# Kernel tuning notes

Hardware: AMD Instinct MI355X
Metric: run time of the kernel (lower is better)

The kernel has to match this reference:

```python
import jax, jax.numpy as jnp
import numpy as np

N_GENES = 2000
D_MODEL = 256
N_LAYERS = 4
D_STATE = 16
D_CONV = 4
EXPAND = 2
D_INNER = EXPAND * D_MODEL  # 512
DT_RANK = (D_MODEL + 15) // 16  # 16


def layer_norm(x, w, b, eps=1e-5):
    mu = jnp.mean(x, axis=-1, keepdims=True)
    var = jnp.mean((x - mu) ** 2, axis=-1, keepdims=True)
    return (x - mu) * jax.lax.rsqrt(var + eps) * w + b


def mamba_mixer(h, in_w, cw, cb, xp_w, dtp_w, dtp_b, A_log, Dvec, out_w):
    # h: [B, L, d_model]
    B, L, _ = h.shape
    xz = jnp.einsum('bld,ed->ble', h, in_w)            # [B,L,2*Di]
    u, z = jnp.split(xz, 2, axis=-1)                    # [B,L,Di] each
    # causal depthwise conv1d (kernel D_CONV)
    up = jnp.pad(u, ((0, 0), (D_CONV - 1, 0), (0, 0)))
    u = sum(up[:, k:k + L, :] * cw[:, k] for k in range(D_CONV)) + cb
    u = jax.nn.silu(u)
    # input-dependent dt, B, C
    xdbc = jnp.einsum('bld,ed->ble', u, xp_w)           # [B,L,dt_rank+2N]
    dt_r = xdbc[..., :DT_RANK]
    Bm = xdbc[..., DT_RANK:DT_RANK + D_STATE]           # [B,L,N]
    Cm = xdbc[..., DT_RANK + D_STATE:]                  # [B,L,N]
    dt = jax.nn.softplus(jnp.einsum('blr,dr->bld', dt_r, dtp_w) + dtp_b)  # [B,L,Di]
    A = -jnp.exp(A_log)                                 # [Di,N]
    dA = jnp.exp(dt[..., None] * A)                     # [B,L,Di,N]
    dBu = dt[..., None] * Bm[:, :, None, :] * u[..., None]

    def step(hst, inp):
        a, bu = inp
        hst = a * hst + bu
        return hst, hst

    h0 = jnp.zeros((B, D_INNER, D_STATE), dA.dtype)
    _, hs = jax.lax.scan(step, h0, (jnp.moveaxis(dA, 1, 0), jnp.moveaxis(dBu, 1, 0)))
    y = jnp.einsum('lbdn,lbn->bld', hs, jnp.moveaxis(Cm, 1, 0)) + u * Dvec
    y = y * jax.nn.silu(z)
    return jnp.einsum('bld,ed->ble', y, out_w)          # [B,L,d_model]


def setup_inputs() -> dict:
    key = jax.random.key(0)
    ks = jax.random.split(key, 16)
    nl = N_LAYERS
    inp = {
        'x': jax.random.normal(ks[0], (2, N_GENES), jnp.float32),
        'bulk_in_w': jax.random.normal(ks[1], (D_MODEL,), jnp.float32),
        'bulk_in_b': jnp.zeros((D_MODEL,), jnp.float32),
        'gene_emb': jax.random.normal(ks[2], (1, N_GENES, D_MODEL), jnp.float32) * 0.02,
        'mod_emb': jax.random.normal(ks[3], (1, 1, D_MODEL), jnp.float32) * 0.02,
        'ln_w': jnp.ones((nl, D_MODEL), jnp.float32),
        'ln_b': jnp.zeros((nl, D_MODEL), jnp.float32),
        'in_proj_w': jax.random.normal(ks[4], (nl, 2 * D_INNER, D_MODEL), jnp.float32) * (D_MODEL ** -0.5),
        'conv_w': jax.random.normal(ks[5], (nl, D_INNER, D_CONV), jnp.float32) * (D_CONV ** -0.5),
        'conv_b': jnp.zeros((nl, D_INNER), jnp.float32),
        'x_proj_w': jax.random.normal(ks[6], (nl, DT_RANK + 2 * D_STATE, D_INNER), jnp.float32) * (D_INNER ** -0.5),
        'dt_proj_w': jax.random.normal(ks[7], (nl, D_INNER, DT_RANK), jnp.float32) * 0.01,
        'dt_proj_b': jnp.full((nl, D_INNER), -4.0, jnp.float32),
        'A_log': jnp.broadcast_to(jnp.log(jnp.arange(1, D_STATE + 1, dtype=jnp.float32)), (nl, D_INNER, D_STATE)).copy(),
        'D': jnp.ones((nl, D_INNER), jnp.float32),
        'out_proj_w': jax.random.normal(ks[8], (nl, D_MODEL, D_INNER), jnp.float32) * (D_INNER ** -0.5),
        'fin_w': jnp.ones((D_MODEL,), jnp.float32),
        'fin_b': jnp.zeros((D_MODEL,), jnp.float32),
        'head_w': jax.random.normal(ks[9], (D_MODEL,), jnp.float32) * (D_MODEL ** -0.5),
        'head_b': jnp.zeros((), jnp.float32),
    }
    return inp


def reference(x, bulk_in_w, bulk_in_b, gene_emb, mod_emb, ln_w, ln_b, in_proj_w,
              conv_w, conv_b, x_proj_w, dt_proj_w, dt_proj_b, A_log, D, out_proj_w,
              fin_w, fin_b, head_w, head_b):
    # token embed (modality='bulk'); Linear(1,d_model) == x[...,None]*w + b
    h = x[..., None] * bulk_in_w + bulk_in_b + gene_emb + mod_emb  # [B,L,d_model]
    for i in range(N_LAYERS):
        h = h + mamba_mixer(layer_norm(h, ln_w[i], ln_b[i]), in_proj_w[i], conv_w[i],
                            conv_b[i], x_proj_w[i], dt_proj_w[i], dt_proj_b[i],
                            A_log[i], D[i], out_proj_w[i])
    h = layer_norm(h, fin_w, fin_b)
    y = jnp.einsum('bld,d->bl', h, head_w) + head_b  # bulk head, squeeze(-1)
    return y
```

## Files before the change

kernel.cpp:

```cpp
#include <hip/hip_runtime.h>
#include <math.h>

#define B_  2
#define L_  2000
#define DM_ 256
#define DI_ 512
#define DS_ 16
#define NL_ 4
#define BL_ (B_*L_)
#define BLP_ 4096
#define NC_  125
#define CL_  16
#define NST_ (B_*DI_*DS_)

#define NF_IP_ (NL_*64*8*64)
#define NF_OP_ (NL_*16*16*64)
#define NF_XP_ (NL_*3*16*64)
#define NF_TOT_ (NF_IP_ + NF_OP_ + NF_XP_)

typedef unsigned short ushort_t;
typedef __attribute__((ext_vector_type(8))) short bf16x8;
typedef __attribute__((ext_vector_type(4))) float f32x4;

__device__ __forceinline__ float siluf(float x) { return x / (1.f + __expf(-x)); }
__device__ __forceinline__ ushort_t f2bf(float x) {
    unsigned int u = __float_as_uint(x);
    return (ushort_t)((u + 0x7FFFu + ((u >> 16) & 1u)) >> 16);
}
__device__ __forceinline__ float bf2f(ushort_t v) {
    return __uint_as_float(((unsigned int)v) << 16);
}

__global__ __launch_bounds__(256) void embed_f2bf_kernel(
    const float* __restrict__ x, const float* __restrict__ biw,
    const float* __restrict__ bib, const float* __restrict__ ge,
    const float* __restrict__ me, const float* __restrict__ lnw,
    const float* __restrict__ lnb,
    float* __restrict__ h, ushort_t* __restrict__ aln,
    const float* __restrict__ ipw, const float* __restrict__ opw,
    const float* __restrict__ xpw, ushort_t* __restrict__ ipwb,
    ushort_t* __restrict__ opwb, ushort_t* __restrict__ xpwb)
{
    if (blockIdx.x < BL_) {
        __shared__ float sm[8];
        int bl = blockIdx.x, d = threadIdx.x;
        int l = bl % L_;
        float v = x[bl]*biw[d] + bib[d] + ge[(size_t)l*DM_ + d] + me[d];
        h[(size_t)bl*DM_ + d] = v;
        float s = v, q = v*v;
        #pragma unroll
        for (int o = 32; o > 0; o >>= 1) {
            s += __shfl_down(s, o);
            q += __shfl_down(q, o);
        }
        if ((d & 63) == 0) { sm[d >> 6] = s; sm[4 + (d >> 6)] = q; }
        __syncthreads();
        float sum = sm[0]+sm[1]+sm[2]+sm[3];
        float ssq = sm[4]+sm[5]+sm[6]+sm[7];
        float mu  = sum * (1.f/DM_);
        float inv = rsqrtf(fmaxf(ssq*(1.f/DM_) - mu*mu, 0.f) + 1e-5f);
        aln[(size_t)bl*DM_ + d] = f2bf((v - mu)*inv*lnw[d] + lnb[d]);
    } else {
        int i = (blockIdx.x - BL_)*256 + threadIdx.x;
        if (i >= NF_TOT_) return;
        const float* src; ushort_t* dst;
        if (i < NF_IP_) {
            int f = i;
            int li   = f >> 15;
            int r    = f & 32767;
            int t    = r >> 9;
            int rem  = r & 511;
            int ks   = rem >> 6;
            int lane = rem & 63;
            src = ipw + ((size_t)(li*1024 + t*16 + (lane & 15)))*DM_
                      + ks*32 + (lane >> 4)*8;
            dst = ipwb + (size_t)f*8;
        } else if (i < NF_IP_ + NF_OP_) {
            int f = i - NF_IP_;
            int li   = f >> 14;
            int r    = f & 16383;
            int t    = r >> 10;
            int rem  = r & 1023;
            int ks   = rem >> 6;
            int lane = rem & 63;
            src = opw + ((size_t)(li*256 + t*16 + (lane & 15)))*DI_
                      + ks*32 + (lane >> 4)*8;
            dst = opwb + (size_t)f*8;
        } else {
            int f = i - NF_IP_ - NF_OP_;
            int li   = f / 3072;
            int r    = f % 3072;
            int t    = r >> 10;
            int rem  = r & 1023;
            int ks   = rem >> 6;
            int lane = rem & 63;
            src = xpw + ((size_t)(li*48 + t*16 + (lane & 15)))*DI_
                      + ks*32 + (lane >> 4)*8;
            dst = xpwb + (size_t)f*8;
        }
        float4 v0 = *(const float4*)src;
        float4 v1 = *(const float4*)(src + 4);
        __align__(16) ushort_t o[8];
        o[0] = f2bf(v0.x); o[1] = f2bf(v0.y); o[2] = f2bf(v0.z); o[3] = f2bf(v0.w);
        o[4] = f2bf(v1.x); o[5] = f2bf(v1.y); o[6] = f2bf(v1.z); o[7] = f2bf(v1.w);
        *(uint4*)dst = *(const uint4*)o;
    }
}

__global__ __launch_bounds__(256) void gemm_bf(
    const ushort_t* __restrict__ A, const ushort_t* __restrict__ Wp,
    ushort_t* __restrict__ C)
{
    __shared__ ushort_t a_s[128*64];
    const int r0 = blockIdx.x*128, c0 = blockIdx.y*128;
    const int tid = threadIdx.x;
    const int lane = tid & 63, w = tid >> 6;
    const int wm = (w & 1)*64, wn = (w >> 1)*64;
    const int qd = lane >> 4, l16 = lane & 15;
    const int tb = (c0 + wn) >> 4;
    f32x4 acc[4][4] = {};
    for (int kc = 0; kc < DM_; kc += 64) {
        #pragma unroll
        for (int q = 0; q < 4; q++) {
            int ch = tid + 256*q;
            int row = ch >> 3, col8 = (ch & 7)*8;
            *(bf16x8*)&a_s[row*64 + col8] =
                *(const bf16x8*)(A + (size_t)(r0 + row)*DM_ + kc + col8);
        }
        __syncthreads();
        #pragma unroll
        for (int ks = 0; ks < 2; ks++) {
            int ksg = (kc >> 5) + ks;
            bf16x8 af[4], bf[4];
            #pragma unroll
            for (int i = 0; i < 4; i++)
                af[i] = *(const bf16x8*)&a_s[(wm + i*16 + l16)*64 + ks*32 + qd*8];
            #pragma unroll
            for (int j = 0; j < 4; j++)
                bf[j] = *(const bf16x8*)(Wp +
                    (((size_t)(tb + j)*8 + ksg)*64 + lane)*8);
            #pragma unroll
            for (int i = 0; i < 4; i++) {
                #pragma unroll
                for (int j = 0; j < 4; j++)
                    acc[i][j] = __builtin_amdgcn_mfma_f32_16x16x32_bf16(
                        af[i], bf[j], acc[i][j], 0, 0, 0);
            }
        }
        __syncthreads();
    }
    #pragma unroll
    for (int i = 0; i < 4; i++) {
        #pragma unroll
        for (int j = 0; j < 4; j++) {
            #pragma unroll
            for (int r = 0; r < 4; r++) {
                int row = r0 + wm + i*16 + qd*4 + r;
                int col = c0 + wn + j*16 + l16;
                C[(size_t)row*1024 + col] = f2bf(acc[i][j][r]);
            }
        }
    }
}

__global__ __launch_bounds__(512) void conv_xproj512(
    const ushort_t* __restrict__ xz, const float* __restrict__ cw,
    const float* __restrict__ cb, const ushort_t* __restrict__ XWp,
    const float* __restrict__ DTW, const float* __restrict__ DTB,
    const float* __restrict__ Alog,
    ushort_t* __restrict__ u_bf, float* __restrict__ bn,
    float* __restrict__ cn, ushort_t* __restrict__ dtn,
    float2* __restrict__ sa)
{
    __shared__ ushort_t xs[19][520];
    __shared__ ushort_t us[16][520];
    __shared__ float ps[8*768];
    __shared__ float dtr_s[16][16];
    const int c = blockIdx.x, b = blockIdx.y, l0 = c*CL_;
    const int tid = threadIdx.x;
    const int lane = tid & 63, w = tid >> 6;
    const int qd = lane >> 4, l16 = lane & 15;
    for (int f = tid; f < 19*64; f += 512) {
        int row = f >> 6, c8 = (f & 63)*8;
        int l = l0 - 3 + row;
        uint4 v = {0u,0u,0u,0u};
        if (l >= 0) v = *(const uint4*)(xz + (size_t)(b*L_ + l)*1024 + c8);
        *(uint4*)&xs[row][c8] = v;
    }
    __syncthreads();
    {
        int ch = tid;
        float4 wv = *(const float4*)(cw + ch*4);
        float bias = cb[ch];
        float x0 = bf2f(xs[0][ch]);
        float x1 = bf2f(xs[1][ch]);
        float x2 = bf2f(xs[2][ch]);
        #pragma unroll
        for (int j = 0; j < 16; j++) {
            float x3 = bf2f(xs[3 + j][ch]);
            float v = fmaf(x0, wv.x, fmaf(x1, wv.y, fmaf(x2, wv.z, fmaf(x3, wv.w, bias))));
            us[j][ch] = f2bf(siluf(v));
            x0 = x1; x1 = x2; x2 = x3;
        }
    }
    __syncthreads();
    for (int f = tid; f < 16*64; f += 512) {
        int row = f >> 6, c8 = (f & 63)*8;
        *(uint4*)(u_bf + (size_t)(b*L_ + l0 + row)*512 + c8) =
            *(const uint4*)&us[row][c8];
    }
    f32x4 acc[3] = {};
    #pragma unroll
    for (int st = 0; st < 2; st++) {
        int k = w*64 + st*32 + qd*8;
        int ksg = w*2 + st;
        bf16x8 af = *(const bf16x8*)&us[l16][k];
        #pragma unroll
        for (int j = 0; j < 3; j++) {
            bf16x8 bv = *(const bf16x8*)(XWp +
                (((size_t)j*16 + ksg)*64 + lane)*8);
            acc[j] = __builtin_amdgcn_mfma_f32_16x16x32_bf16(af, bv, acc[j], 0, 0, 0);
        }
    }
    #pragma unroll
    for (int j = 0; j < 3; j++)
        #pragma unroll
        for (int r = 0; r < 4; r++)
            ps[w*768 + (qd*4 + r)*48 + j*16 + l16] = acc[j][r];
    __syncthreads();
    for (int e = tid; e < 768; e += 512) {
        float v = ps[e] + ps[768+e] + ps[1536+e] + ps[2304+e]
                + ps[3072+e] + ps[3840+e] + ps[4608+e] + ps[5376+e];
        ps[e] = v;
    }
    __syncthreads();
    if (tid < 256) {
        int row = tid >> 4, n = tid & 15;
        dtr_s[row][n] = ps[row*48 + n];
        size_t base = ((size_t)(b*L_) + l0 + row)*DS_ + n;
        bn[base] = ps[row*48 + 16 + n];
        cn[base] = ps[row*48 + 32 + n];
    }
    __syncthreads();
    {
        const int d = tid;
        float wreg[16];
        const float4* wp = (const float4*)(DTW + (size_t)d*16);
        #pragma unroll
        for (int k4 = 0; k4 < 4; k4++) {
            float4 v = wp[k4];
            wreg[4*k4+0] = v.x; wreg[4*k4+1] = v.y;
            wreg[4*k4+2] = v.z; wreg[4*k4+3] = v.w;
        }
        float bias = DTB[d];
        float dtv[16];
        #pragma unroll
        for (int r = 0; r < 16; r++) {
            float a = bias;
            #pragma unroll
            for (int k = 0; k < 16; k++) a = fmaf(dtr_s[r][k], wreg[k], a);
            float dt = a > 20.f ? a : log1pf(__expf(a));
            ushort_t dtb16 = f2bf(dt);
            dtn[((size_t)(b*L_) + l0 + r)*DI_ + d] = dtb16;
            dtv[r] = bf2f(dtb16);
        }
        float Ac[DS_], s[DS_], ap[DS_];
        const float* ar = Alog + (size_t)d*DS_;
        #pragma unroll
        for (int n = 0; n < DS_; n++) { Ac[n] = -__expf(ar[n]); s[n] = 0.f; ap[n] = 1.f; }
        #pragma unroll
        for (int l = 0; l < 16; l++) {
            float dt = dtv[l];
            float u  = bf2f(us[l][d]);
            float dtu = dt*u;
            #pragma unroll
            for (int n = 0; n < DS_; n++) {
                float e = __expf(dt*Ac[n]);
                s[n] = fmaf(e, s[n], dtu*ps[l*48 + 16 + n]);
                ap[n] *= e;
            }
        }
        size_t ib = (((size_t)c*B_ + b)*DI_ + d)*DS_;
        float2* sap = sa + ib;
        #pragma unroll
        for (int k = 0; k < 8; k++)
            *(float4*)&sap[2*k] = make_float4(s[2*k], ap[2*k], s[2*k+1], ap[2*k+1]);
    }
}

__global__ __launch_bounds__(64) void scan_phase2(
    const float2* __restrict__ sa, float* __restrict__ sinc)
{
    const int t = blockIdx.x*64 + threadIdx.x;
    float s = 0.f;
    for (int g = 0; g < 5; g++) {
        float2 v[25];
        #pragma unroll
        for (int i = 0; i < 25; i++)
            v[i] = sa[(size_t)(g*25 + i)*NST_ + t];
        #pragma unroll
        for (int i = 0; i < 25; i++) {
            sinc[(size_t)(g*25 + i)*NST_ + t] = s;
            s = fmaf(v[i].y, s, v[i].x);
        }
    }
}

template<int LAST>
__global__ __launch_bounds__(512) void phase3_fused(
    const ushort_t* __restrict__ dtn, const ushort_t* __restrict__ u_bf,
    const float* __restrict__ bn, const float* __restrict__ cn,
    const float* __restrict__ Alog, const float* __restrict__ Dv,
    const float* __restrict__ sinc, const ushort_t* __restrict__ xz,
    const ushort_t* __restrict__ opw, float* __restrict__ h,
    const float* __restrict__ lnw, const float* __restrict__ lnb,
    const ushort_t* __restrict__ ipw, ushort_t* __restrict__ xz_out,
    const float* __restrict__ hw, const float* __restrict__ hb,
    float* __restrict__ out)
{
    __shared__ float b_sh[CL_*DS_];
    __shared__ float c_sh[CL_*DS_];
    __shared__ ushort_t ys[16][520];
    __shared__ union { ushort_t dt_t[16][520]; ushort_t z_t[16][520]; } T0;
    __shared__ union { ushort_t u_t[16][520];  ushort_t a_sh[16][264]; } T1;
    __shared__ float2 red2[128];
    __shared__ float2 muv[16];
    const int c = blockIdx.x, b = blockIdx.y, l0 = c*CL_;
    const int tid = threadIdx.x;
    const int w = tid >> 6, lane = tid & 63;
    const int qd = lane >> 4, l16 = lane & 15;
    {
        int f = tid & 255;
        size_t src = ((size_t)(b*L_) + l0)*DS_ + f;
        if (tid < 256) b_sh[f] = bn[src];
        else           c_sh[f] = cn[src];
    }
    {
        const int r = tid >> 5, cb16 = (tid & 31)*16;
        size_t rb = ((size_t)(b*L_) + l0 + r)*DI_ + cb16;
        *(uint4*)&T0.dt_t[r][cb16]     = *(const uint4*)(dtn + rb);
        *(uint4*)&T0.dt_t[r][cb16 + 8] = *(const uint4*)(dtn + rb + 8);
        *(uint4*)&T1.u_t[r][cb16]      = *(const uint4*)(u_bf + rb);
        *(uint4*)&T1.u_t[r][cb16 + 8]  = *(const uint4*)(u_bf + rb + 8);
    }
    const int d = tid;
    float Ac[DS_], s[DS_];
    {
        const float* ar = Alog + (size_t)d*DS_;
        #pragma unroll
        for (int n = 0; n < DS_; n++) Ac[n] = -__expf(ar[n]);
        size_t base = (((size_t)c*B_ + b)*DI_ + d)*DS_;
        #pragma unroll
        for (int n4 = 0; n4 < 4; n4++)
            *(float4*)&s[4*n4] = *(const float4*)(sinc + base + 4*n4);
    }
    const float Dd = Dv[d];
    __syncthreads();
    float y_reg[CL_];
    #pragma unroll
    for (int l = 0; l < CL_; l++) {
        float dt = bf2f(T0.dt_t[l][d]);
        float u  = bf2f(T1.u_t[l][d]);
        float dtu = dt*u;
        float y = u*Dd;
        #pragma unroll
        for (int n = 0; n < DS_; n++) {
            float e = __expf(dt*Ac[n]);
            s[n] = fmaf(e, s[n], dtu*b_sh[l*DS_ + n]);
            y = fmaf(s[n], c_sh[l*DS_ + n], y);
        }
        y_reg[l] = y;
    }
    __syncthreads();
    {
        const int r = tid >> 5, cb16 = (tid & 31)*16;
        size_t rb = ((size_t)(b*L_) + l0 + r)*1024 + 512 + cb16;
        *(uint4*)&T0.z_t[r][cb16]     = *(const uint4*)(xz + rb);
        *(uint4*)&T0.z_t[r][cb16 + 8] = *(const uint4*)(xz + rb + 8);
    }
    __syncthreads();
    #pragma unroll
    for (int l = 0; l < CL_; l++)
        ys[l][d] = f2bf(y_reg[l] * siluf(bf2f(T0.z_t[l][d])));
    __syncthreads();
    f32x4 acc[2] = {};
    #pragma unroll
    for (int ks = 0; ks < 16; ks++) {
        bf16x8 af = *(const bf16x8*)&ys[l16][ks*32 + qd*8];
        #pragma unroll
        for (int j = 0; j < 2; j++) {
            bf16x8 bv = *(const bf16x8*)(opw +
                (((size_t)(w*2 + j)*16 + ks)*64 + lane)*8);
            acc[j] = __builtin_amdgcn_mfma_f32_16x16x32_bf16(af, bv, acc[j], 0, 0, 0);
        }
    }
    float v[2][4];
    #pragma unroll
    for (int r = 0; r < 4; r++) {
        int lrow = qd*4 + r;
        size_t gr = (size_t)(b*L_ + l0 + lrow);
        float sm = 0.f, sq = 0.f;
        #pragma unroll
        for (int j = 0; j < 2; j++) {
            int col = w*32 + j*16 + l16;
            size_t idx = gr*DM_ + col;
            float vv = h[idx] + acc[j][r];
            if (!LAST) h[idx] = vv;
            v[j][r] = vv;
            sm += vv; sq += vv*vv;
        }
        sm += __shfl_xor(sm, 1); sq += __shfl_xor(sq, 1);
        sm += __shfl_xor(sm, 2); sq += __shfl_xor(sq, 2);
        sm += __shfl_xor(sm, 4); sq += __shfl_xor(sq, 4);
        sm += __shfl_xor(sm, 8); sq += __shfl_xor(sq, 8);
        if (l16 == 0) red2[w*16 + lrow] = make_float2(sm, sq);
    }
    __syncthreads();
    if (tid < 16) {
        float sm = 0.f, sq = 0.f;
        #pragma unroll
        for (int ww = 0; ww < 8; ww++) {
            float2 t = red2[ww*16 + tid];
            sm += t.x; sq += t.y;
        }
        float mu  = sm*(1.f/DM_);
        float inv = rsqrtf(fmaxf(sq*(1.f/DM_) - mu*mu, 0.f) + 1e-5f);
        muv[tid] = make_float2(mu, inv);
    }
    __syncthreads();
    if (!LAST) {
        #pragma unroll
        for (int r = 0; r < 4; r++) {
            int lrow = qd*4 + r;
            float2 mi = muv[lrow];
            #pragma unroll
            for (int j = 0; j < 2; j++) {
                int col = w*32 + j*16 + l16;
                T1.a_sh[lrow][col] = f2bf((v[j][r] - mi.x)*mi.y*lnw[col] + lnb[col]);
            }
        }
        __syncthreads();
        f32x4 acc2[8] = {};
        const int n0 = w*128;
        #pragma unroll
        for (int ks = 0; ks < 8; ks++) {
            bf16x8 af = *(const bf16x8*)&T1.a_sh[l16][ks*32 + qd*8];
            #pragma unroll
            for (int j2 = 0; j2 < 8; j2++) {
                bf16x8 bv = *(const bf16x8*)(ipw +
                    (((size_t)(w*8 + j2)*8 + ks)*64 + lane)*8);
                acc2[j2] = __builtin_amdgcn_mfma_f32_16x16x32_bf16(af, bv, acc2[j2], 0, 0, 0);
            }
        }
        #pragma unroll
        for (int j2 = 0; j2 < 8; j2++) {
            #pragma unroll
            for (int r = 0; r < 4; r++) {
                size_t row = (size_t)(b*L_ + l0 + qd*4 + r);
                xz_out[row*1024 + n0 + j2*16 + l16] = f2bf(acc2[j2][r]);
            }
        }
    } else {
        float hd[4];
        #pragma unroll
        for (int r = 0; r < 4; r++) {
            int lrow = qd*4 + r;
            float2 mi = muv[lrow];
            float aa = 0.f;
            #pragma unroll
            for (int j = 0; j < 2; j++) {
                int col = w*32 + j*16 + l16;
                float nv = (v[j][r] - mi.x)*mi.y*lnw[col] + lnb[col];
                aa = fmaf(nv, hw[col], aa);
            }
            hd[r] = aa;
        }
        #pragma unroll
        for (int r = 0; r < 4; r++) {
            float xv = hd[r];
            xv += __shfl_xor(xv, 1); xv += __shfl_xor(xv, 2);
            xv += __shfl_xor(xv, 4); xv += __shfl_xor(xv, 8);
            if (l16 == 0) red2[w*16 + qd*4 + r].x = xv;
        }
        __syncthreads();
        if (tid < 16) {
            float xv = 0.f;
            #pragma unroll
            for (int ww = 0; ww < 8; ww++) xv += red2[ww*16 + tid].x;
            out[(size_t)(b*L_) + l0 + tid] = xv + hb[0];
        }
    }
}

extern "C" void kernel_launch(void* const* d_in, const int* in_sizes, int n_in,
                              void* d_out, int out_size, void* d_ws, size_t ws_size,
                              hipStream_t stream)
{
    const float* x    = (const float*)d_in[0];
    const float* biw  = (const float*)d_in[1];
    const float* bib  = (const float*)d_in[2];
    const float* ge   = (const float*)d_in[3];
    const float* me   = (const float*)d_in[4];
    const float* lnw  = (const float*)d_in[5];
    const float* lnb  = (const float*)d_in[6];
    const float* ipw  = (const float*)d_in[7];
    const float* cw   = (const float*)d_in[8];
    const float* cb   = (const float*)d_in[9];
    const float* xpw  = (const float*)d_in[10];
    const float* dtw  = (const float*)d_in[11];
    const float* dtb  = (const float*)d_in[12];
    const float* alog = (const float*)d_in[13];
    const float* Dv   = (const float*)d_in[14];
    const float* opw  = (const float*)d_in[15];
    const float* fw   = (const float*)d_in[16];
    const float* fb   = (const float*)d_in[17];
    const float* hw   = (const float*)d_in[18];
    const float* hb   = (const float*)d_in[19];
    float* out = (float*)d_out;

    float* ws  = (float*)d_ws;
    float* h      = ws;
    float* bn     = h + (size_t)BLP_*DM_;
    float* cn     = bn + (size_t)B_*L_*DS_;
    float2* sa    = (float2*)(cn + (size_t)B_*L_*DS_);
    float* sinc   = (float*)(sa + (size_t)NC_*NST_);
    ushort_t* aln   = (ushort_t*)(sinc + (size_t)NC_*NST_);
    ushort_t* xz_bf = aln + (size_t)BLP_*DM_;
    ushort_t* u_bf  = xz_bf + (size_t)BLP_*1024;
    ushort_t* dtn   = u_bf + (size_t)BLP_*DI_;
    ushort_t* ipwb  = dtn + (size_t)B_*L_*DI_;
    ushort_t* opwb  = ipwb + (size_t)NL_*1024*DM_;
    ushort_t* xpwb  = opwb + (size_t)NL_*DM_*DI_;

    const int conv_blocks = (NF_TOT_ + 255)/256;
    embed_f2bf_kernel<<<BL_ + conv_blocks, 256, 0, stream>>>(
        x, biw, bib, ge, me, lnw, lnb, h, aln,
        ipw, opw, xpw, ipwb, opwb, xpwb);

    gemm_bf<<<dim3(BLP_/128, 1024/128), 256, 0, stream>>>(
        aln, ipwb, xz_bf);

    for (int i = 0; i < NL_; i++) {
        conv_xproj512<<<dim3(NC_, B_), 512, 0, stream>>>(
            xz_bf, cw + i*DI_*4, cb + i*DI_, xpwb + (size_t)i*48*512,
            dtw + (size_t)i*DI_*16, dtb + i*DI_, alog + (size_t)i*DI_*DS_,
            u_bf, bn, cn, dtn, sa);
        scan_phase2<<<NST_/64, 64, 0, stream>>>(sa, sinc);
        if (i < NL_-1) {
            phase3_fused<0><<<dim3(NC_, B_), 512, 0, stream>>>(
                dtn, u_bf, bn, cn, alog + (size_t)i*DI_*DS_, Dv + i*DI_,
                sinc, xz_bf, opwb + (size_t)i*DM_*DI_, h,
                lnw + (i+1)*DM_, lnb + (i+1)*DM_,
                ipwb + (size_t)(i+1)*1024*DM_, xz_bf,
                nullptr, nullptr, nullptr);
        } else {
            phase3_fused<1><<<dim3(NC_, B_), 512, 0, stream>>>(
                dtn, u_bf, bn, cn, alog + (size_t)i*DI_*DS_, Dv + i*DI_,
                sinc, xz_bf, opwb + (size_t)i*DM_*DI_, h,
                fw, fb,
                nullptr, xz_bf,
                hw, hb, out);
        }
    }
}
```

Measured before the change: 354.9 us.

## Halve scan chunk length to eight rows, doubling blocks per kernel

```diff
diff --git a/kernel.cpp b/kernel.cpp
--- a/kernel.cpp
+++ b/kernel.cpp
@@ -9,8 +9,8 @@
 #define NL_ 4
 #define BL_ (B_*L_)
 #define BLP_ 4096
-#define NC_  125
-#define CL_  16
+#define CL_  8
+#define NC_  250
 #define NST_ (B_*DI_*DS_)
 
 #define NF_IP_ (NL_*64*8*64)
@@ -172,15 +172,20 @@
     float* __restrict__ cn, ushort_t* __restrict__ dtn,
     float2* __restrict__ sa)
 {
-    __shared__ ushort_t xs[19][520];
+    __shared__ ushort_t xs[11][520];
     __shared__ ushort_t us[16][520];
-    __shared__ float ps[8*768];
-    __shared__ float dtr_s[16][16];
+    __shared__ float ps[8*384];
+    __shared__ float dtr_s[8][16];
     const int c = blockIdx.x, b = blockIdx.y, l0 = c*CL_;
     const int tid = threadIdx.x;
     const int lane = tid & 63, w = tid >> 6;
     const int qd = lane >> 4, l16 = lane & 15;
-    for (int f = tid; f < 19*64; f += 512) {
+    {
+        int row = 8 + (tid >> 6), c8 = (tid & 63)*8;
+        uint4 z = {0u,0u,0u,0u};
+        *(uint4*)&us[row][c8] = z;
+    }
+    for (int f = tid; f < 11*64; f += 512) {
         int row = f >> 6, c8 = (f & 63)*8;
         int l = l0 - 3 + row;
         uint4 v = {0u,0u,0u,0u};
@@ -196,7 +201,7 @@
         float x1 = bf2f(xs[1][ch]);
         float x2 = bf2f(xs[2][ch]);
         #pragma unroll
-        for (int j = 0; j < 16; j++) {
+        for (int j = 0; j < CL_; j++) {
             float x3 = bf2f(xs[3 + j][ch]);
             float v = fmaf(x0, wv.x, fmaf(x1, wv.y, fmaf(x2, wv.z, fmaf(x3, wv.w, bias))));
             us[j][ch] = f2bf(siluf(v));
@@ -204,8 +209,8 @@
         }
     }
     __syncthreads();
-    for (int f = tid; f < 16*64; f += 512) {
-        int row = f >> 6, c8 = (f & 63)*8;
+    {
+        int row = tid >> 6, c8 = (tid & 63)*8;
         *(uint4*)(u_bf + (size_t)(b*L_ + l0 + row)*512 + c8) =
             *(const uint4*)&us[row][c8];
     }
@@ -225,16 +230,18 @@
     #pragma unroll
     for (int j = 0; j < 3; j++)
         #pragma unroll
-        for (int r = 0; r < 4; r++)
-            ps[w*768 + (qd*4 + r)*48 + j*16 + l16] = acc[j][r];
-    __syncthreads();
-    for (int e = tid; e < 768; e += 512) {
-        float v = ps[e] + ps[768+e] + ps[1536+e] + ps[2304+e]
-                + ps[3072+e] + ps[3840+e] + ps[4608+e] + ps[5376+e];
+        for (int r = 0; r < 4; r++) {
+            int row = qd*4 + r;
+            if (row < 8) ps[w*384 + row*48 + j*16 + l16] = acc[j][r];
+        }
+    __syncthreads();
+    for (int e = tid; e < 384; e += 512) {
+        float v = ps[e] + ps[384+e] + ps[768+e] + ps[1152+e]
+                + ps[1536+e] + ps[1920+e] + ps[2304+e] + ps[2688+e];
         ps[e] = v;
     }
     __syncthreads();
-    if (tid < 256) {
+    if (tid < 128) {
         int row = tid >> 4, n = tid & 15;
         dtr_s[row][n] = ps[row*48 + n];
         size_t base = ((size_t)(b*L_) + l0 + row)*DS_ + n;
@@ -253,9 +260,9 @@
             wreg[4*k4+2] = v.z; wreg[4*k4+3] = v.w;
         }
         float bias = DTB[d];
-        float dtv[16];
-        #pragma unroll
-        for (int r = 0; r < 16; r++) {
+        float dtv[CL_];
+        #pragma unroll
+        for (int r = 0; r < CL_; r++) {
             float a = bias;
             #pragma unroll
             for (int k = 0; k < 16; k++) a = fmaf(dtr_s[r][k], wreg[k], a);
@@ -269,7 +276,7 @@
         #pragma unroll
         for (int n = 0; n < DS_; n++) { Ac[n] = -__expf(ar[n]); s[n] = 0.f; ap[n] = 1.f; }
         #pragma unroll
-        for (int l = 0; l < 16; l++) {
+        for (int l = 0; l < CL_; l++) {
             float dt = dtv[l];
             float u  = bf2f(us[l][d]);
             float dtu = dt*u;
@@ -293,7 +300,7 @@
 {
     const int t = blockIdx.x*64 + threadIdx.x;
     float s = 0.f;
-    for (int g = 0; g < 5; g++) {
+    for (int g = 0; g < 10; g++) {
         float2 v[25];
         #pragma unroll
         for (int i = 0; i < 25; i++)
@@ -321,27 +328,26 @@
     __shared__ float b_sh[CL_*DS_];
     __shared__ float c_sh[CL_*DS_];
     __shared__ ushort_t ys[16][520];
-    __shared__ union { ushort_t dt_t[16][520]; ushort_t z_t[16][520]; } T0;
-    __shared__ union { ushort_t u_t[16][520];  ushort_t a_sh[16][264]; } T1;
-    __shared__ float2 red2[128];
-    __shared__ float2 muv[16];
+    __shared__ union { ushort_t dt_t[8][520]; ushort_t z_t[8][520]; } T0;
+    __shared__ union { ushort_t u_t[8][520];  ushort_t a_sh[16][264]; } T1;
+    __shared__ float2 red2[64];
+    __shared__ float2 muv[8];
     const int c = blockIdx.x, b = blockIdx.y, l0 = c*CL_;
     const int tid = threadIdx.x;
     const int w = tid >> 6, lane = tid & 63;
     const int qd = lane >> 4, l16 = lane & 15;
-    {
-        int f = tid & 255;
-        size_t src = ((size_t)(b*L_) + l0)*DS_ + f;
-        if (tid < 256) b_sh[f] = bn[src];
-        else           c_sh[f] = cn[src];
-    }
-    {
-        const int r = tid >> 5, cb16 = (tid & 31)*16;
-        size_t rb = ((size_t)(b*L_) + l0 + r)*DI_ + cb16;
-        *(uint4*)&T0.dt_t[r][cb16]     = *(const uint4*)(dtn + rb);
-        *(uint4*)&T0.dt_t[r][cb16 + 8] = *(const uint4*)(dtn + rb + 8);
-        *(uint4*)&T1.u_t[r][cb16]      = *(const uint4*)(u_bf + rb);
-        *(uint4*)&T1.u_t[r][cb16 + 8]  = *(const uint4*)(u_bf + rb + 8);
+    if (tid < 128)       b_sh[tid]       = bn[((size_t)(b*L_) + l0)*DS_ + tid];
+    else if (tid < 256)  c_sh[tid - 128] = cn[((size_t)(b*L_) + l0)*DS_ + (tid - 128)];
+    {
+        int row = 8 + (tid >> 6), c8 = (tid & 63)*8;
+        uint4 z = {0u,0u,0u,0u};
+        *(uint4*)&ys[row][c8] = z;
+    }
+    {
+        const int r = tid >> 6, cb8 = (tid & 63)*8;
+        size_t rb = ((size_t)(b*L_) + l0 + r)*DI_ + cb8;
+        *(uint4*)&T0.dt_t[r][cb8] = *(const uint4*)(dtn + rb);
+        *(uint4*)&T1.u_t[r][cb8]  = *(const uint4*)(u_bf + rb);
     }
     const int d = tid;
     float Ac[DS_], s[DS_];
@@ -373,10 +379,14 @@
     }
     __syncthreads();
     {
-        const int r = tid >> 5, cb16 = (tid & 31)*16;
-        size_t rb = ((size_t)(b*L_) + l0 + r)*1024 + 512 + cb16;
-        *(uint4*)&T0.z_t[r][cb16]     = *(const uint4*)(xz + rb);
-        *(uint4*)&T0.z_t[r][cb16 + 8] = *(const uint4*)(xz + rb + 8);
+        const int r = tid >> 6, cb8 = (tid & 63)*8;
+        size_t rb = ((size_t)(b*L_) + l0 + r)*1024 + 512 + cb8;
+        *(uint4*)&T0.z_t[r][cb8] = *(const uint4*)(xz + rb);
+    }
+    if (tid < 256) {
+        int row = 8 + (tid >> 5), c8 = (tid & 31)*8;
+        uint4 z = {0u,0u,0u,0u};
+        *(uint4*)&T1.a_sh[row][c8] = z;
     }
     __syncthreads();
     #pragma unroll
@@ -398,29 +408,31 @@
     #pragma unroll
     for (int r = 0; r < 4; r++) {
         int lrow = qd*4 + r;
-        size_t gr = (size_t)(b*L_ + l0 + lrow);
+        if (lrow < 8) {
+            size_t gr = (size_t)(b*L_ + l0 + lrow);
+            float sm = 0.f, sq = 0.f;
+            #pragma unroll
+            for (int j = 0; j < 2; j++) {
+                int col = w*32 + j*16 + l16;
+                size_t idx = gr*DM_ + col;
+                float vv = h[idx] + acc[j][r];
+                if (!LAST) h[idx] = vv;
+                v[j][r] = vv;
+                sm += vv; sq += vv*vv;
+            }
+            sm += __shfl_xor(sm, 1); sq += __shfl_xor(sq, 1);
+            sm += __shfl_xor(sm, 2); sq += __shfl_xor(sq, 2);
+            sm += __shfl_xor(sm, 4); sq += __shfl_xor(sq, 4);
+            sm += __shfl_xor(sm, 8); sq += __shfl_xor(sq, 8);
+            if (l16 == 0) red2[w*8 + lrow] = make_float2(sm, sq);
+        }
+    }
+    __syncthreads();
+    if (tid < 8) {
         float sm = 0.f, sq = 0.f;
         #pragma unroll
-        for (int j = 0; j < 2; j++) {
-            int col = w*32 + j*16 + l16;
-            size_t idx = gr*DM_ + col;
-            float vv = h[idx] + acc[j][r];
-            if (!LAST) h[idx] = vv;
-            v[j][r] = vv;
-            sm += vv; sq += vv*vv;
-        }
-        sm += __shfl_xor(sm, 1); sq += __shfl_xor(sq, 1);
-        sm += __shfl_xor(sm, 2); sq += __shfl_xor(sq, 2);
-        sm += __shfl_xor(sm, 4); sq += __shfl_xor(sq, 4);
-        sm += __shfl_xor(sm, 8); sq += __shfl_xor(sq, 8);
-        if (l16 == 0) red2[w*16 + lrow] = make_float2(sm, sq);
-    }
-    __syncthreads();
-    if (tid < 16) {
-        float sm = 0.f, sq = 0.f;
-        #pragma unroll
         for (int ww = 0; ww < 8; ww++) {
-            float2 t = red2[ww*16 + tid];
+            float2 t = red2[ww*8 + tid];
             sm += t.x; sq += t.y;
         }
         float mu  = sm*(1.f/DM_);
@@ -432,11 +444,13 @@
         #pragma unroll
         for (int r = 0; r < 4; r++) {
             int lrow = qd*4 + r;
-            float2 mi = muv[lrow];
-            #pragma unroll
-            for (int j = 0; j < 2; j++) {
-                int col = w*32 + j*16 + l16;
-                T1.a_sh[lrow][col] = f2bf((v[j][r] - mi.x)*mi.y*lnw[col] + lnb[col]);
+            if (lrow < 8) {
+                float2 mi = muv[lrow];
+                #pragma unroll
+                for (int j = 0; j < 2; j++) {
+                    int col = w*32 + j*16 + l16;
+                    T1.a_sh[lrow][col] = f2bf((v[j][r] - mi.x)*mi.y*lnw[col] + lnb[col]);
+                }
             }
         }
         __syncthreads();
@@ -456,8 +470,11 @@
         for (int j2 = 0; j2 < 8; j2++) {
             #pragma unroll
             for (int r = 0; r < 4; r++) {
-                size_t row = (size_t)(b*L_ + l0 + qd*4 + r);
-                xz_out[row*1024 + n0 + j2*16 + l16] = f2bf(acc2[j2][r]);
+                int lrow = qd*4 + r;
+                if (lrow < 8) {
+                    size_t row = (size_t)(b*L_ + l0 + lrow);
+                    xz_out[row*1024 + n0 + j2*16 + l16] = f2bf(acc2[j2][r]);
+                }
             }
         }
     } else {
@@ -465,28 +482,33 @@
         #pragma unroll
         for (int r = 0; r < 4; r++) {
             int lrow = qd*4 + r;
-            float2 mi = muv[lrow];
-            float aa = 0.f;
-            #pragma unroll
-            for (int j = 0; j < 2; j++) {
-                int col = w*32 + j*16 + l16;
-                float nv = (v[j][r] - mi.x)*mi.y*lnw[col] + lnb[col];
-                aa = fmaf(nv, hw[col], aa);
-            }
-            hd[r] = aa;
+            if (lrow < 8) {
+                float2 mi = muv[lrow];
+                float aa = 0.f;
+                #pragma unroll
+                for (int j = 0; j < 2; j++) {
+                    int col = w*32 + j*16 + l16;
+                    float nv = (v[j][r] - mi.x)*mi.y*lnw[col] + lnb[col];
+                    aa = fmaf(nv, hw[col], aa);
+                }
+                hd[r] = aa;
+            }
         }
         #pragma unroll
         for (int r = 0; r < 4; r++) {
-            float xv = hd[r];
-            xv += __shfl_xor(xv, 1); xv += __shfl_xor(xv, 2);
-            xv += __shfl_xor(xv, 4); xv += __shfl_xor(xv, 8);
-            if (l16 == 0) red2[w*16 + qd*4 + r].x = xv;
+            int lrow = qd*4 + r;
+            if (lrow < 8) {
+                float xv = hd[r];
+                xv += __shfl_xor(xv, 1); xv += __shfl_xor(xv, 2);
+                xv += __shfl_xor(xv, 4); xv += __shfl_xor(xv, 8);
+                if (l16 == 0) red2[w*8 + lrow].x = xv;
+            }
         }
         __syncthreads();
-        if (tid < 16) {
+        if (tid < 8) {
             float xv = 0.f;
             #pragma unroll
-            for (int ww = 0; ww < 8; ww++) xv += red2[ww*16 + tid].x;
+            for (int ww = 0; ww < 8; ww++) xv += red2[ww*8 + tid].x;
             out[(size_t)(b*L_) + l0 + tid] = xv + hb[0];
         }
     }
```

New measurement: 382.3 us. 1.08x slower.
